# Optimization experiments

Hardware: AMD Instinct MI355X
Metric: run time of the kernel (lower is better)

## Reference

```python
import jax, jax.numpy as jnp
import numpy as np

B, L, D = 32, 512, 1024

def setup_inputs() -> dict:
    key = jax.random.key(0)
    ks = jax.random.split(key, 9)
    s = 0.02
    return {
        "query": jax.random.normal(ks[0], (B, L, D), jnp.float32),
        "context": jax.random.normal(ks[1], (B, L, D), jnp.float32),
        "W_in": jax.random.normal(ks[2], (D, D), jnp.float32) * s,
        "b_in": jax.random.normal(ks[3], (D,), jnp.float32) * s,
        "W_in2": jax.random.normal(ks[4], (D, D), jnp.float32) * s,
        "b_in2": jax.random.normal(ks[5], (D,), jnp.float32) * s,
        "W_out": jax.random.normal(ks[6], (L, D), jnp.float32) * s,  # windows_lens == L
        "W_fc": jax.random.normal(ks[7], (D, 2 * D), jnp.float32) * s,
        "b_fc": jax.random.normal(ks[8], (D,), jnp.float32) * s,
    }

def reference(query, context, W_in, b_in, W_in2, b_in2, W_out, W_fc, b_fc):
    # additive (Bahdanau) score: tanh(Wq q + Wc c) @ W_out^T -> [B, L, L]
    q = jnp.einsum('bld,ed->ble', query, W_in) + b_in
    c = jnp.einsum('bld,ed->ble', context, W_in2) + b_in2
    alpha = jnp.einsum('bld,wd->blw', jnp.tanh(q + c), W_out)  # [B, L, L]
    alpha = jax.nn.softmax(alpha, axis=-1)
    mix = jnp.einsum('blw,bwd->bld', alpha, context)           # bmm
    cat = jnp.concatenate([mix, context], axis=-1)             # [B, L, 2D]
    out = jnp.einsum('blf,df->bld', cat, W_fc) + b_fc
    return out, alpha
```

## Files before the change

kernel.cpp:

```cpp
#include <hip/hip_runtime.h>
#include <hip/hip_bf16.h>
#include <cstdint>

typedef unsigned short u16;
typedef unsigned int u32;
typedef __bf16 bf16x8 __attribute__((ext_vector_type(8)));
typedef float f32x4 __attribute__((ext_vector_type(4)));
typedef u16 u16x8 __attribute__((ext_vector_type(8)));

#define DEVINL __device__ __forceinline__

typedef __attribute__((address_space(1))) const u32 gbl_u32;
typedef __attribute__((address_space(3))) u32 lds_u32;

DEVINL void llds16(const void* g, void* l) {
  __builtin_amdgcn_global_load_lds((gbl_u32*)g, (lds_u32*)l, 16, 0, 0);
}

DEVINL u16 f2bf(float f) {
  union { float f; u32 i; } x; x.f = f;
  u32 r = x.i + 0x7FFFu + ((x.i >> 16) & 1u);
  return (u16)(r >> 16);
}

DEVINL float fast_tanh(float x) {
  x = fminf(10.f, fmaxf(-10.f, x));
  float e = __expf(2.f * x);
  return (e - 1.f) / (e + 1.f);
}

DEVINL bf16x8 cvt8(const float4& a, const float4& b) {
  bf16x8 r;
  r[0] = (__bf16)a.x; r[1] = (__bf16)a.y; r[2] = (__bf16)a.z; r[3] = (__bf16)a.w;
  r[4] = (__bf16)b.x; r[5] = (__bf16)b.y; r[6] = (__bf16)b.z; r[7] = (__bf16)b.w;
  return r;
}

__global__ __launch_bounds__(256) void cvtk(const float* __restrict__ src,
                                            u16* __restrict__ dst, int n8) {
  int i = blockIdx.x * 256 + threadIdx.x;
  if (i >= n8) return;
  const float* s = src + (size_t)i * 8;
  *(bf16x8*)(dst + (size_t)i * 8) = cvt8(*(const float4*)s, *(const float4*)(s + 4));
}

__global__ __launch_bounds__(256) void tile_b(const float* __restrict__ src,
                                              int srcld, int koff,
                                              u16* __restrict__ dst, int nchunks) {
  int id = blockIdx.x * 256 + threadIdx.x;
  if (id >= nchunks) return;
  int n = id >> 7, k8 = id & 127;
  int kb = k8 >> 2, h = k8 & 3;
  int u = h * 128 + ((n & 127) ^ (h << 1));
  const float* s = src + (size_t)n * srcld + koff + k8 * 8;
  size_t dc = ((size_t)((n >> 7) * 32 + kb) * 512 + u) * 8;
  *(bf16x8*)(dst + dc) = cvt8(*(const float4*)s, *(const float4*)(s + 4));
}

__global__ __launch_bounds__(256) void tile_b64(const float* __restrict__ src,
                                                int srcld, int koff,
                                                u16* __restrict__ dst, int nchunks) {
  int id = blockIdx.x * 256 + threadIdx.x;
  if (id >= nchunks) return;
  int n = id >> 7, k8 = id & 127;
  int kb = k8 >> 3, h = k8 & 7;
  int u = h * 256 + ((n & 255) ^ (h << 1));
  const float* s = src + (size_t)n * srcld + koff + k8 * 8;
  size_t dc = ((size_t)((n >> 8) * 16 + kb) * 2048 + u) * 8;
  *(bf16x8*)(dst + dc) = cvt8(*(const float4*)s, *(const float4*)(s + 4));
}

template <int NSEG, bool OUT_BF16, bool TANH>
__global__ __launch_bounds__(512) void gemm_nt9(
    const u16* __restrict__ A0, const u16* __restrict__ A1,
    const u16* __restrict__ Bt0, const u16* __restrict__ Bt1,
    const float* __restrict__ bias0, const float* __restrict__ bias1,
    void* __restrict__ Cout, int ldc) {
  __shared__ u16 As[3][16384];
  __shared__ u16 Bs[2][16384];
  const int tid = threadIdx.x, lane = tid & 63, w = tid >> 6;
  const int wr = w >> 2, wc = w & 3;

  const int NX = gridDim.x;
  const int total = NX * gridDim.y;
  const int flat = blockIdx.y * NX + blockIdx.x;
  const int wid = (flat & 7) * (total >> 3) + (flat >> 3);
  const int nb = wid % NX;
  const int n0 = nb * 256, m0 = (wid / NX) * 256;

  f32x4 acc[8][4];
#pragma unroll
  for (int i = 0; i < 8; ++i)
#pragma unroll
    for (int j = 0; j < 4; ++j) acc[i][j] = (f32x4)0.f;

  u32 asrc[4], bofs[4];
#pragma unroll
  for (int r = 0; r < 4; ++r) {
    int u = r * 512 + w * 64 + lane;
    int row = u >> 3, oct = (u & 7) ^ (row & 7);
    asrc[r] = (u32)(m0 + row) * 1024u + (u32)(oct * 8);
    bofs[r] = (u32)u * 8u;
  }

  const int NT = NSEG * 16;

  auto stageA = [&](int t) {
    const int seg = (NSEG == 2 && t >= 16) ? 1 : 0;
    const int kb = t - (seg << 4);
    const u16* Ap = seg ? A1 : A0;
    const u32 k0 = (u32)(kb << 6);
    u16* dst = As[t % 3];
#pragma unroll
    for (int q = 0; q < 4; ++q)
      llds16(Ap + (size_t)(asrc[q] + k0), dst + (q * 512 + w * 64) * 8);
  };
  auto stageB = [&](int t) {
    const int seg = (NSEG == 2 && t >= 16) ? 1 : 0;
    const int kb = t - (seg << 4);
    const u16* Bt = (seg ? Bt1 : Bt0) + ((size_t)(nb * 16 + kb) << 14);
    u16* dst = Bs[t & 1];
#pragma unroll
    for (int q = 0; q < 4; ++q)
      llds16(Bt + (size_t)bofs[q], dst + (q * 512 + w * 64) * 8);
  };

  stageA(0);
  stageB(0);
  if (NT > 1) stageA(1);

  const int rl = lane & 15;
  for (int t = 0; t < NT; ++t) {
    const int ab = t % 3, bb = t & 1;
    const bool preB = (t + 1 < NT);
    const bool preA = (t + 2 < NT);

    if (preB) asm volatile("s_waitcnt vmcnt(6)" ::: "memory");
    else      asm volatile("s_waitcnt vmcnt(2)" ::: "memory");
    __builtin_amdgcn_s_barrier();
    __builtin_amdgcn_sched_barrier(0);
    {
      const int h = lane >> 4;
      const int jA = h ^ (rl & 7);
      bf16x8 af[8], bv[4];
#pragma unroll
      for (int i = 0; i < 8; ++i)
        af[i] = *(const bf16x8*)&As[ab][((wr * 128 + i * 16 + rl) * 8 + jA) * 8];
#pragma unroll
      for (int j = 0; j < 4; ++j)
        bv[j] = *(const bf16x8*)&Bs[bb][(h * 256 + ((wc * 64 + j * 16 + rl) ^ (h << 1))) * 8];
      if (preB) stageB(t + 1);
      __builtin_amdgcn_s_setprio(1);
#pragma unroll
      for (int i = 0; i < 8; ++i)
#pragma unroll
        for (int j = 0; j < 4; ++j)
          acc[i][j] =
              __builtin_amdgcn_mfma_f32_16x16x32_bf16(af[i], bv[j], acc[i][j], 0, 0, 0);
      __builtin_amdgcn_s_setprio(0);
    }
    if (preB) asm volatile("s_waitcnt vmcnt(8)" ::: "memory");
    else      asm volatile("s_waitcnt vmcnt(0)" ::: "memory");
    __builtin_amdgcn_s_barrier();
    __builtin_amdgcn_sched_barrier(0);
    {
      const int h = 4 + (lane >> 4);
      const int jA = h ^ (rl & 7);
      bf16x8 af[8], bv[4];
#pragma unroll
      for (int i = 0; i < 8; ++i)
        af[i] = *(const bf16x8*)&As[ab][((wr * 128 + i * 16 + rl) * 8 + jA) * 8];
#pragma unroll
      for (int j = 0; j < 4; ++j)
        bv[j] = *(const bf16x8*)&Bs[bb][(h * 256 + ((wc * 64 + j * 16 + rl) ^ (h << 1))) * 8];
      if (preA) stageA(t + 2);
      __builtin_amdgcn_s_setprio(1);
#pragma unroll
      for (int i = 0; i < 8; ++i)
#pragma unroll
        for (int j = 0; j < 4; ++j)
          acc[i][j] =
              __builtin_amdgcn_mfma_f32_16x16x32_bf16(af[i], bv[j], acc[i][j], 0, 0, 0);
      __builtin_amdgcn_s_setprio(0);
    }
  }

  const int rq = lane >> 4;
#pragma unroll
  for (int j = 0; j < 4; ++j) {
    const int gc = n0 + wc * 64 + j * 16 + rl;
    float bia = 0.f;
    if (bias0) bia += bias0[gc];
    if (NSEG == 2 && bias1) bia += bias1[gc];
#pragma unroll
    for (int i = 0; i < 8; ++i) {
#pragma unroll
      for (int r = 0; r < 4; ++r) {
        const int grow = m0 + wr * 128 + i * 16 + rq * 4 + r;
        float v = acc[i][j][r] + bia;
        if (TANH) v = fast_tanh(v);
        if (OUT_BF16)
          ((u16*)Cout)[(size_t)grow * ldc + gc] = f2bf(v);
        else
          ((float*)Cout)[(size_t)grow * ldc + gc] = v;
      }
    }
  }
}

template <int NSEG, bool OUT_BF16, bool TANH>
__global__ __launch_bounds__(256) void gemm_nt4(
    const u16* __restrict__ A0, const u16* __restrict__ A1, int lda,
    const u16* __restrict__ Bt0, const u16* __restrict__ Bt1,
    const float* __restrict__ bias0, const float* __restrict__ bias1,
    void* __restrict__ Cout, int ldc) {
  __shared__ u16 As[2][4096];
  __shared__ u16 Bs[2][4096];
  const int tid = threadIdx.x, lane = tid & 63, w = tid >> 6;
  const int wr = w >> 1, wc = w & 1;
  const int NX = gridDim.x;
  const int total = NX * gridDim.y;
  const int flat = blockIdx.y * NX + blockIdx.x;
  const int wid = (flat & 7) * (total >> 3) + (flat >> 3);
  const int nb = wid % NX;
  const int n0 = nb * 128, m0 = (wid / NX) * 128;
  const int h = lane >> 4, rl = lane & 15;
  const int jA = h ^ (rl & 3);

  f32x4 acc[4][4];
#pragma unroll
  for (int i = 0; i < 4; ++i)
#pragma unroll
    for (int j = 0; j < 4; ++j) acc[i][j] = (f32x4)0.f;

  const int gb0 = w * 64, gb1 = 256 + w * 64;
  u32 asrc[2];
  {
    int u0 = gb0 + lane, u1 = gb1 + lane;
    int r0 = u0 >> 2, o0 = (u0 & 3) ^ (r0 & 3);
    int r1 = u1 >> 2, o1 = (u1 & 3) ^ (r1 & 3);
    asrc[0] = (u32)(m0 + r0) * (u32)lda + (u32)(o0 * 8);
    asrc[1] = (u32)(m0 + r1) * (u32)lda + (u32)(o1 * 8);
  }
  const int NT = NSEG * 32;

  auto stage = [&](int t, int buf) {
    const int seg = (NSEG == 2 && t >= 32) ? 1 : 0;
    const int kb = t - seg * 32, kl = kb << 5;
    {
      const u16* Bt = (seg ? Bt1 : Bt0) + ((size_t)(nb * 32 + kb) * 512) * 8;
      llds16(Bt + (size_t)(gb0 + lane) * 8, &Bs[buf][gb0 * 8]);
      llds16(Bt + (size_t)(gb1 + lane) * 8, &Bs[buf][gb1 * 8]);
    }
    {
      const u16* Ap = seg ? A1 : A0;
      llds16(Ap + (size_t)(asrc[0] + kl), &As[buf][gb0 * 8]);
      llds16(Ap + (size_t)(asrc[1] + kl), &As[buf][gb1 * 8]);
    }
  };
  auto compute = [&](int buf) {
    bf16x8 af[4], bfv[4];
#pragma unroll
    for (int i = 0; i < 4; ++i)
      af[i] = *(const bf16x8*)&As[buf][((wr * 64 + i * 16 + rl) * 4 + jA) * 8];
#pragma unroll
    for (int j = 0; j < 4; ++j)
      bfv[j] = *(const bf16x8*)&Bs[buf][(h * 128 + ((wc * 64 + j * 16 + rl) ^ (h << 1))) * 8];
#pragma unroll
    for (int i = 0; i < 4; ++i)
#pragma unroll
      for (int j = 0; j < 4; ++j)
        acc[i][j] =
            __builtin_amdgcn_mfma_f32_16x16x32_bf16(af[i], bfv[j], acc[i][j], 0, 0, 0);
  };

  stage(0, 0);
  for (int t = 0; t < NT; ++t) {
    const int c = t & 1;
    if (t + 1 < NT) {
      stage(t + 1, c ^ 1);
      asm volatile("s_waitcnt vmcnt(4)" ::: "memory");
    } else {
      asm volatile("s_waitcnt vmcnt(0)" ::: "memory");
    }
    __builtin_amdgcn_s_barrier();
    __builtin_amdgcn_sched_barrier(0);
    compute(c);
    __builtin_amdgcn_s_barrier();
  }

  const int rq = lane >> 4;
#pragma unroll
  for (int j = 0; j < 4; ++j) {
    const int gc = n0 + wc * 64 + j * 16 + rl;
    float bia = 0.f;
    if (bias0) bia += bias0[gc];
    if (NSEG == 2 && bias1) bia += bias1[gc];
#pragma unroll
    for (int i = 0; i < 4; ++i) {
#pragma unroll
      for (int r = 0; r < 4; ++r) {
        const int grow = m0 + wr * 64 + i * 16 + rq * 4 + r;
        float v = acc[i][j][r] + bia;
        if (TANH) v = fast_tanh(v);
        if (OUT_BF16)
          ((u16*)Cout)[(size_t)grow * ldc + gc] = f2bf(v);
        else
          ((float*)Cout)[(size_t)grow * ldc + gc] = v;
      }
    }
  }
}

__global__ __launch_bounds__(256) void gemm_nn3(
    const float* __restrict__ alpha, const u16* __restrict__ ctxb,
    u16* __restrict__ mix) {
  __shared__ u16 As[2][4096];
  __shared__ u16 Bs[2][4096];
  const int tid = threadIdx.x, lane = tid & 63, w = tid >> 6;
  const int wr = w >> 1, wc = w & 1;
  const int b = blockIdx.z;
  const int n0 = blockIdx.x * 128, m0 = blockIdx.y * 128;
  const int h = lane >> 4, rlx = (lane & 15) ^ (h << 1);
  const float* A = alpha + (size_t)b * 262144;
  u16* C = mix + (size_t)b * 524288;

  f32x4 acc[4][4];
#pragma unroll
  for (int i = 0; i < 4; ++i)
#pragma unroll
    for (int j = 0; j < 4; ++j) acc[i][j] = (f32x4)0.f;

  const int row0 = tid >> 2, cb = tid & 3, row1 = 64 + row0;
  const int unit0 = cb * 128 + (row0 ^ (cb << 1));
  const int unit1 = cb * 128 + (row1 ^ (cb << 1));
  const int kl = tid & 31, ng = tid >> 5;
  const int hb = kl >> 3, kp = kl & 7;

  float4 fr[4];
  u16x8 ub[2];

  auto stage = [&](int t) {
    const int k0 = t << 5;
    const float* p0 = A + (size_t)(m0 + row0) * 512 + k0 + cb * 8;
    const float* p1 = A + (size_t)(m0 + row1) * 512 + k0 + cb * 8;
    fr[0] = *(const float4*)p0; fr[1] = *(const float4*)(p0 + 4);
    fr[2] = *(const float4*)p1; fr[3] = *(const float4*)(p1 + 4);
    const u16* Cb = ctxb + (size_t)b * 524288 + (size_t)(k0 + kl) * 1024 +
                    n0 + ng * 16;
    ub[0] = *(const u16x8*)Cb; ub[1] = *(const u16x8*)(Cb + 8);
  };
  auto stage_fin = [&](int buf) {
    *(bf16x8*)&As[buf][unit0 * 8] = cvt8(fr[0], fr[1]);
    *(bf16x8*)&As[buf][unit1 * 8] = cvt8(fr[2], fr[3]);
#pragma unroll
    for (int j = 0; j < 16; ++j) {
      int n = ng * 16 + j;
      Bs[buf][(hb * 128 + (n ^ (hb << 1))) * 8 + kp] =
          (j < 8) ? ub[0][j] : ub[1][j - 8];
    }
  };
  auto compute = [&](int buf) {
    bf16x8 af[4], bfv[4];
#pragma unroll
    for (int i = 0; i < 4; ++i)
      af[i] = *(const bf16x8*)&As[buf][(h * 128 + wr * 64 + i * 16 + rlx) * 8];
#pragma unroll
    for (int j = 0; j < 4; ++j)
      bfv[j] = *(const bf16x8*)&Bs[buf][(h * 128 + wc * 64 + j * 16 + rlx) * 8];
#pragma unroll
    for (int i = 0; i < 4; ++i)
#pragma unroll
      for (int j = 0; j < 4; ++j)
        acc[i][j] =
            __builtin_amdgcn_mfma_f32_16x16x32_bf16(af[i], bfv[j], acc[i][j], 0, 0, 0);
  };

  stage(0);
  stage_fin(0);
  __syncthreads();
  for (int t = 0; t < 16; ++t) {
    const int cb_ = t & 1;
    if (t + 1 < 16) stage(t + 1);
    compute(cb_);
    if (t + 1 < 16) stage_fin(cb_ ^ 1);
    __syncthreads();
  }

  const int rl = lane & 15, rq = lane >> 4;
#pragma unroll
  for (int j = 0; j < 4; ++j) {
    const int gc = n0 + wc * 64 + j * 16 + rl;
#pragma unroll
    for (int i = 0; i < 4; ++i) {
#pragma unroll
      for (int r = 0; r < 4; ++r) {
        const int grow = m0 + wr * 64 + i * 16 + rq * 4 + r;
        C[(size_t)grow * 1024 + gc] = f2bf(acc[i][j][r]);
      }
    }
  }
}

__global__ __launch_bounds__(256) void softmax_rows_f32(float* __restrict__ S) {
  const int row = blockIdx.x * 4 + (threadIdx.x >> 6);
  const int lane = threadIdx.x & 63;
  float* s = S + (size_t)row * 512 + lane * 8;
  float4 v0 = *(const float4*)s;
  float4 v1 = *(const float4*)(s + 4);
  float vs[8] = {v0.x, v0.y, v0.z, v0.w, v1.x, v1.y, v1.z, v1.w};
  float vm = vs[0];
#pragma unroll
  for (int j = 1; j < 8; ++j) vm = fmaxf(vm, vs[j]);
#pragma unroll
  for (int off = 32; off > 0; off >>= 1) vm = fmaxf(vm, __shfl_xor(vm, off, 64));
  float e[8];
  float sum = 0.f;
#pragma unroll
  for (int j = 0; j < 8; ++j) { e[j] = __expf(vs[j] - vm); sum += e[j]; }
#pragma unroll
  for (int off = 32; off > 0; off >>= 1) sum += __shfl_xor(sum, off, 64);
  float inv = 1.f / sum;
  float4 o0 = {e[0] * inv, e[1] * inv, e[2] * inv, e[3] * inv};
  float4 o1 = {e[4] * inv, e[5] * inv, e[6] * inv, e[7] * inv};
  *(float4*)s = o0;
  *(float4*)(s + 4) = o1;
}

extern "C" void kernel_launch(void* const* d_in, const int* in_sizes, int n_in,
                              void* d_out, int out_size, void* d_ws, size_t ws_size,
                              hipStream_t stream) {
  const float* query = (const float*)d_in[0];
  const float* ctx   = (const float*)d_in[1];
  const float* W_in  = (const float*)d_in[2];
  const float* b_in  = (const float*)d_in[3];
  const float* W_in2 = (const float*)d_in[4];
  const float* b_in2 = (const float*)d_in[5];
  const float* W_out = (const float*)d_in[6];
  const float* W_fc  = (const float*)d_in[7];
  const float* b_fc  = (const float*)d_in[8];

  float* out   = (float*)d_out;
  float* alpha = (float*)d_out + 16777216;

  u16* wibf_t  = (u16*)d_ws;
  u16* wi2bf_t = wibf_t + 1048576;
  u16* wobf_t  = wibf_t + 2097152;
  u16* wf0_t   = wibf_t + 2621440;
  u16* wf1_t   = wibf_t + 3670016;
  u16* t_ws    = (u16*)((char*)d_ws + 9437184);
  u16* cbf     = (u16*)((char*)d_ws + 42991616);
  u16* qbf     = (u16*)((char*)d_ws + 76546048);

  dim3 blk(256, 1, 1);
  dim3 blk5(512, 1, 1);

  tile_b64<<<dim3(512), blk, 0, stream>>>(W_in, 1024, 0, wibf_t, 131072);
  tile_b64<<<dim3(512), blk, 0, stream>>>(W_in2, 1024, 0, wi2bf_t, 131072);
  tile_b<<<dim3(256), blk, 0, stream>>>(W_out, 1024, 0, wobf_t, 65536);
  tile_b64<<<dim3(512), blk, 0, stream>>>(W_fc, 2048, 0, wf0_t, 131072);
  tile_b64<<<dim3(512), blk, 0, stream>>>(W_fc, 2048, 1024, wf1_t, 131072);
  cvtk<<<dim3(8192), blk, 0, stream>>>(ctx, cbf, 2097152);
  cvtk<<<dim3(8192), blk, 0, stream>>>(query, qbf, 2097152);

  gemm_nt9<2, true, true><<<dim3(4, 64), blk5, 0, stream>>>(
      qbf, cbf, wibf_t, wi2bf_t, b_in, b_in2, t_ws, 1024);

  gemm_nt4<1, false, false><<<dim3(4, 128), blk, 0, stream>>>(
      t_ws, nullptr, 1024, wobf_t, nullptr, nullptr, nullptr, alpha, 512);

  softmax_rows_f32<<<dim3(4096), blk, 0, stream>>>(alpha);

  gemm_nn3<<<dim3(8, 4, 32), blk, 0, stream>>>(alpha, cbf, t_ws);

  gemm_nt9<2, false, false><<<dim3(4, 64), blk5, 0, stream>>>(
      t_ws, cbf, wf0_t, wf1_t, b_fc, nullptr, out, 1024);
}
```

Measured before the change: 285.9 us.

## Split GEMM K-step into four interleaved phases with finer-grained load staging

Restructures the main loop of the 256x256 bf16 GEMM so that each half K-step is split into two MFMA phases over pairs of B columns. Each phase reads only two B fragments and issues half of the next tile's global-to-LDS copies. Barriers and vmcnt waits are redistributed across four points per iteration. The aim is to interleave LDS reads, async loads and MFMA work more finely, in the style of a ping-pong schedule. The cost is more barriers per iteration, plus the risk of mismatched waitcnt accounting.

```diff
diff --git a/kernel.cpp b/kernel.cpp
--- a/kernel.cpp
+++ b/kernel.cpp
@@ -71,7 +71,7 @@
 }
 
 template <int NSEG, bool OUT_BF16, bool TANH>
-__global__ __launch_bounds__(512) void gemm_nt9(
+__global__ __launch_bounds__(512) void gemm_nt10(
     const u16* __restrict__ A0, const u16* __restrict__ A1,
     const u16* __restrict__ Bt0, const u16* __restrict__ Bt1,
     const float* __restrict__ bias0, const float* __restrict__ bias1,
@@ -115,6 +115,18 @@
     for (int q = 0; q < 4; ++q)
       llds16(Ap + (size_t)(asrc[q] + k0), dst + (q * 512 + w * 64) * 8);
   };
+  auto stageA2 = [&](int t, int rp) {
+    const int seg = (NSEG == 2 && t >= 16) ? 1 : 0;
+    const int kb = t - (seg << 4);
+    const u16* Ap = seg ? A1 : A0;
+    const u32 k0 = (u32)(kb << 6);
+    u16* dst = As[t % 3];
+#pragma unroll
+    for (int r = 0; r < 2; ++r) {
+      const int q = rp * 2 + r;
+      llds16(Ap + (size_t)(asrc[q] + k0), dst + (q * 512 + w * 64) * 8);
+    }
+  };
   auto stageB = [&](int t) {
     const int seg = (NSEG == 2 && t >= 16) ? 1 : 0;
     const int kb = t - (seg << 4);
@@ -124,63 +136,106 @@
     for (int q = 0; q < 4; ++q)
       llds16(Bt + (size_t)bofs[q], dst + (q * 512 + w * 64) * 8);
   };
+  auto stageB2 = [&](int t, int rp) {
+    const int seg = (NSEG == 2 && t >= 16) ? 1 : 0;
+    const int kb = t - (seg << 4);
+    const u16* Bt = (seg ? Bt1 : Bt0) + ((size_t)(nb * 16 + kb) << 14);
+    u16* dst = Bs[t & 1];
+#pragma unroll
+    for (int r = 0; r < 2; ++r) {
+      const int q = rp * 2 + r;
+      llds16(Bt + (size_t)bofs[q], dst + (q * 512 + w * 64) * 8);
+    }
+  };
 
   stageA(0);
   stageB(0);
   if (NT > 1) stageA(1);
+  asm volatile("s_waitcnt vmcnt(6)" ::: "memory");
+  __builtin_amdgcn_s_barrier();
 
   const int rl = lane & 15;
   for (int t = 0; t < NT; ++t) {
     const int ab = t % 3, bb = t & 1;
     const bool preB = (t + 1 < NT);
     const bool preA = (t + 2 < NT);
-
-    if (preB) asm volatile("s_waitcnt vmcnt(6)" ::: "memory");
-    else      asm volatile("s_waitcnt vmcnt(2)" ::: "memory");
-    __builtin_amdgcn_s_barrier();
-    __builtin_amdgcn_sched_barrier(0);
+    bf16x8 af[8];
+
     {
       const int h = lane >> 4;
       const int jA = h ^ (rl & 7);
-      bf16x8 af[8], bv[4];
 #pragma unroll
       for (int i = 0; i < 8; ++i)
         af[i] = *(const bf16x8*)&As[ab][((wr * 128 + i * 16 + rl) * 8 + jA) * 8];
-#pragma unroll
-      for (int j = 0; j < 4; ++j)
-        bv[j] = *(const bf16x8*)&Bs[bb][(h * 256 + ((wc * 64 + j * 16 + rl) ^ (h << 1))) * 8];
-      if (preB) stageB(t + 1);
+      bf16x8 b0 = *(const bf16x8*)&Bs[bb][(h * 256 + ((wc * 64 + 0 + rl) ^ (h << 1))) * 8];
+      bf16x8 b1 = *(const bf16x8*)&Bs[bb][(h * 256 + ((wc * 64 + 16 + rl) ^ (h << 1))) * 8];
+      if (preB) stageB2(t + 1, 0);
+      __builtin_amdgcn_s_barrier();
+      asm volatile("s_waitcnt lgkmcnt(0)" ::: "memory");
+      __builtin_amdgcn_sched_barrier(0);
       __builtin_amdgcn_s_setprio(1);
 #pragma unroll
-      for (int i = 0; i < 8; ++i)
-#pragma unroll
-        for (int j = 0; j < 4; ++j)
-          acc[i][j] =
-              __builtin_amdgcn_mfma_f32_16x16x32_bf16(af[i], bv[j], acc[i][j], 0, 0, 0);
+      for (int i = 0; i < 8; ++i) {
+        acc[i][0] = __builtin_amdgcn_mfma_f32_16x16x32_bf16(af[i], b0, acc[i][0], 0, 0, 0);
+        acc[i][1] = __builtin_amdgcn_mfma_f32_16x16x32_bf16(af[i], b1, acc[i][1], 0, 0, 0);
+      }
       __builtin_amdgcn_s_setprio(0);
     }
-    if (preB) asm volatile("s_waitcnt vmcnt(8)" ::: "memory");
-    else      asm volatile("s_waitcnt vmcnt(0)" ::: "memory");
-    __builtin_amdgcn_s_barrier();
-    __builtin_amdgcn_sched_barrier(0);
+    {
+      const int h = lane >> 4;
+      bf16x8 b2 = *(const bf16x8*)&Bs[bb][(h * 256 + ((wc * 64 + 32 + rl) ^ (h << 1))) * 8];
+      bf16x8 b3 = *(const bf16x8*)&Bs[bb][(h * 256 + ((wc * 64 + 48 + rl) ^ (h << 1))) * 8];
+      if (preB) stageB2(t + 1, 1);
+      if (preB) asm volatile("s_waitcnt vmcnt(8)" ::: "memory");
+      else      asm volatile("s_waitcnt vmcnt(0)" ::: "memory");
+      __builtin_amdgcn_s_barrier();
+      asm volatile("s_waitcnt lgkmcnt(0)" ::: "memory");
+      __builtin_amdgcn_sched_barrier(0);
+      __builtin_amdgcn_s_setprio(1);
+#pragma unroll
+      for (int i = 0; i < 8; ++i) {
+        acc[i][2] = __builtin_amdgcn_mfma_f32_16x16x32_bf16(af[i], b2, acc[i][2], 0, 0, 0);
+        acc[i][3] = __builtin_amdgcn_mfma_f32_16x16x32_bf16(af[i], b3, acc[i][3], 0, 0, 0);
+      }
+      __builtin_amdgcn_s_setprio(0);
+    }
     {
       const int h = 4 + (lane >> 4);
       const int jA = h ^ (rl & 7);
-      bf16x8 af[8], bv[4];
 #pragma unroll
       for (int i = 0; i < 8; ++i)
         af[i] = *(const bf16x8*)&As[ab][((wr * 128 + i * 16 + rl) * 8 + jA) * 8];
-#pragma unroll
-      for (int j = 0; j < 4; ++j)
-        bv[j] = *(const bf16x8*)&Bs[bb][(h * 256 + ((wc * 64 + j * 16 + rl) ^ (h << 1))) * 8];
-      if (preA) stageA(t + 2);
+      bf16x8 b0 = *(const bf16x8*)&Bs[bb][(h * 256 + ((wc * 64 + 0 + rl) ^ (h << 1))) * 8];
+      bf16x8 b1 = *(const bf16x8*)&Bs[bb][(h * 256 + ((wc * 64 + 16 + rl) ^ (h << 1))) * 8];
+      if (preA) stageA2(t + 2, 0);
+      __builtin_amdgcn_s_barrier();
+      asm volatile("s_waitcnt lgkmcnt(0)" ::: "memory");
+      __builtin_amdgcn_sched_barrier(0);
       __builtin_amdgcn_s_setprio(1);
 #pragma unroll
-      for (int i = 0; i < 8; ++i)
-#pragma unroll
-        for (int j = 0; j < 4; ++j)
-          acc[i][j] =
-              __builtin_amdgcn_mfma_f32_16x16x32_bf16(af[i], bv[j], acc[i][j], 0, 0, 0);
+      for (int i = 0; i < 8; ++i) {
+        acc[i][0] = __builtin_amdgcn_mfma_f32_16x16x32_bf16(af[i], b0, acc[i][0], 0, 0, 0);
+        acc[i][1] = __builtin_amdgcn_mfma_f32_16x16x32_bf16(af[i], b1, acc[i][1], 0, 0, 0);
+      }
+      __builtin_amdgcn_s_setprio(0);
+    }
+    {
+      const int h = 4 + (lane >> 4);
+      bf16x8 b2 = *(const bf16x8*)&Bs[bb][(h * 256 + ((wc * 64 + 32 + rl) ^ (h << 1))) * 8];
+      bf16x8 b3 = *(const bf16x8*)&Bs[bb][(h * 256 + ((wc * 64 + 48 + rl) ^ (h << 1))) * 8];
+      if (preA) stageA2(t + 2, 1);
+      if (t < NT - 2)       asm volatile("s_waitcnt vmcnt(6)" ::: "memory");
+      else if (t == NT - 2) asm volatile("s_waitcnt vmcnt(2)" ::: "memory");
+      else                  asm volatile("s_waitcnt vmcnt(0)" ::: "memory");
+      __builtin_amdgcn_s_barrier();
+      asm volatile("s_waitcnt lgkmcnt(0)" ::: "memory");
+      __builtin_amdgcn_sched_barrier(0);
+      __builtin_amdgcn_s_setprio(1);
+#pragma unroll
+      for (int i = 0; i < 8; ++i) {
+        acc[i][2] = __builtin_amdgcn_mfma_f32_16x16x32_bf16(af[i], b2, acc[i][2], 0, 0, 0);
+        acc[i][3] = __builtin_amdgcn_mfma_f32_16x16x32_bf16(af[i], b3, acc[i][3], 0, 0, 0);
+      }
       __builtin_amdgcn_s_setprio(0);
     }
   }
@@ -463,7 +518,7 @@
   cvtk<<<dim3(8192), blk, 0, stream>>>(ctx, cbf, 2097152);
   cvtk<<<dim3(8192), blk, 0, stream>>>(query, qbf, 2097152);
 
-  gemm_nt9<2, true, true><<<dim3(4, 64), blk5, 0, stream>>>(
+  gemm_nt10<2, true, true><<<dim3(4, 64), blk5, 0, stream>>>(
       qbf, cbf, wibf_t, wi2bf_t, b_in, b_in2, t_ws, 1024);
 
   gemm_nt4<1, false, false><<<dim3(4, 128), blk, 0, stream>>>(
@@ -473,6 +528,6 @@
 
   gemm_nn3<<<dim3(8, 4, 32), blk, 0, stream>>>(alpha, cbf, t_ws);
 
-  gemm_nt9<2, false, false><<<dim3(4, 64), blk5, 0, stream>>>(
+  gemm_nt10<2, false, false><<<dim3(4, 64), blk5, 0, stream>>>(
       t_ws, cbf, wf0_t, wf1_t, b_fc, nullptr, out, 1024);
 }
```

New measurement: 284.4 us. No clear change (-0.5%).
